# Performance work log

Hardware: AMD Instinct MI355X
Metric: run time of the kernel (lower is better)

## Reference

```python
import jax, jax.numpy as jnp
import numpy as np

N_NODES = 50000
N_EDGES = 1600000
LORA_R = 8


def gcn_conv(h, W, b, src, dst, n):
    # PyG GCNConv: linear transform, add self-loops, symmetric normalization,
    # scatter-add aggregation at target nodes, then bias.
    h = h @ W  # [N, out]
    ones = jnp.ones(src.shape[0], dtype=h.dtype)
    deg = jax.ops.segment_sum(ones, dst, num_segments=n) + 1.0  # +1 for self-loop
    dis = jax.lax.rsqrt(deg)  # deg >= 1 always
    norm = dis[src] * dis[dst]  # [E]
    agg = jax.ops.segment_sum(norm[:, None] * h[src], dst, num_segments=n)
    agg = agg + (dis * dis)[:, None] * h  # self-loop contribution
    return agg + b


def lora(h, A, B):
    # LoRALinear: b(a(x)) * (1/r); replaces input (not additive)
    return (h @ A) @ B * (1.0 / LORA_R)


def setup_inputs() -> dict:
    key = jax.random.key(0)
    ks = jax.random.split(key, 12)
    inp = {}
    inp['x'] = jax.random.normal(ks[0], (N_NODES, 128), dtype=jnp.float32)
    inp['edge_index'] = jax.random.randint(ks[1], (2, N_EDGES), 0, N_NODES, dtype=jnp.int64 if jax.config.jax_enable_x64 else jnp.int32)
    inp['domain_idx'] = jax.random.randint(ks[2], (N_NODES,), 0, 3, dtype=jnp.int32)
    inp['emb_table'] = jax.random.normal(ks[3], (3, 4096), dtype=jnp.float32)
    s1 = 1.0 / np.sqrt(4224.0)
    inp['W1'] = jax.random.normal(ks[4], (4224, 32), dtype=jnp.float32) * s1
    inp['b1'] = jnp.zeros((32,), dtype=jnp.float32)
    inp['A1'] = jax.random.normal(ks[5], (32, LORA_R), dtype=jnp.float32) * (1.0 / np.sqrt(32.0))
    inp['B1'] = jax.random.normal(ks[6], (LORA_R, 32), dtype=jnp.float32) * (1.0 / np.sqrt(LORA_R))
    inp['W2'] = jax.random.normal(ks[7], (32, 5), dtype=jnp.float32) * (1.0 / np.sqrt(32.0))
    inp['b2'] = jnp.zeros((5,), dtype=jnp.float32)
    inp['A2'] = jax.random.normal(ks[8], (5, LORA_R), dtype=jnp.float32) * (1.0 / np.sqrt(5.0))
    inp['B2'] = jax.random.normal(ks[9], (LORA_R, 5), dtype=jnp.float32) * (1.0 / np.sqrt(LORA_R))
    return inp


def reference(x, edge_index, domain_idx, emb_table, W1, b1, A1, B1, W2, b2, A2, B2):
    n = x.shape[0]
    src, dst = edge_index[0], edge_index[1]
    embedded = emb_table[domain_idx]  # [N, 4096]
    h = jnp.concatenate([embedded, x], axis=1)  # [N, 4224]
    h = gcn_conv(h, W1, b1, src, dst, n)
    h = lora(h, A1, B1)
    h = jax.nn.relu(h)
    h = gcn_conv(h, W2, b2, src, dst, n)
    h = lora(h, A2, B2)
    return jax.nn.log_softmax(h, axis=1)
```

## Files before the change

### kernel.cpp

```cpp
#include <hip/hip_runtime.h>
#include <hip/hip_bf16.h>
#include <hip/hip_fp16.h>


#define XDIM 128
#define EMBDIM 4096
#define TB 8192
#define BSH 6
#define BN 64
#define ECAP2 2560

__global__ void __launch_bounds__(256) k_bin(
    const int* __restrict__ src, const int* __restrict__ dst,
    unsigned int* __restrict__ sorted, int* __restrict__ bcur, int e, int ntiles,
    const float* __restrict__ emb, const float* __restrict__ W1,
    float* __restrict__ emb_part,
    const float* __restrict__ A1, const float* __restrict__ A2,
    const float* __restrict__ B2, const float* __restrict__ b1,
    float* __restrict__ M2, float* __restrict__ b1A1) {
    __shared__ unsigned int staged[TB];
    __shared__ int loff[1024], rctr[1024], sbase[1024];
    int t = threadIdx.x;
    if (blockIdx.x >= ntiles) {
        int bx2 = blockIdx.x - ntiles;
        int dm = bx2 >> 5, seg = bx2 & 31;
        const float* er = emb + dm * EMBDIM + seg * 128;
        const float* wr = W1 + (size_t)(seg * 128) * 32;
        int j = t & 31, kk = t >> 5;
        float acc = 0.f;
        for (int k2 = kk; k2 < 128; k2 += 8) acc += er[k2] * wr[k2 * 32 + j];
        float* p = (float*)staged;
        p[kk * 32 + j] = acc;
        __syncthreads();
        if (t < 32) {
            float s = 0.f;
            #pragma unroll
            for (int r = 0; r < 8; ++r) s += p[r * 32 + t];
            emb_part[bx2 * 32 + t] = s;
        }
        if (bx2 == 0) {
            if (t < 25) {
                int c = t / 5, cp = t % 5;
                float s = 0.f;
                #pragma unroll
                for (int r = 0; r < 8; ++r) s += A2[c * 8 + r] * B2[r * 5 + cp];
                M2[c * 5 + cp] = s * 0.125f;
            }
            if (t >= 32 && t < 40) {
                int j2 = t - 32;
                float s = 0.f;
                #pragma unroll
                for (int k = 0; k < 32; ++k) s += b1[k] * A1[k * 8 + j2];
                b1A1[j2] = s;
            }
        }
        return;
    }
    int base = blockIdx.x * TB;
    int len = min(TB, e - base);
    for (int i = t; i < 1024; i += 256) { loff[i] = 0; rctr[i] = 0; }
    __syncthreads();
    for (int i = t; i < len; i += 256) atomicAdd(&loff[dst[base + i] >> BSH], 1);
    __syncthreads();
    if (t < 64) {
        int ch = t * 16;
        int v[16]; int s0 = 0;
        #pragma unroll
        for (int k = 0; k < 16; ++k) { v[k] = loff[ch + k]; s0 += v[k]; }
        int pre = s0;
        #pragma unroll
        for (int d2 = 1; d2 < 64; d2 <<= 1) {
            int up = __shfl_up(pre, d2);
            if (t >= d2) pre += up;
        }
        int excl = pre - s0;
        #pragma unroll
        for (int k = 0; k < 16; ++k) { loff[ch + k] = excl; excl += v[k]; }
    }
    __syncthreads();
    for (int i = t; i < len; i += 256) {
        int s = src[base + i], d = dst[base + i];
        int b = d >> BSH;
        int r = atomicAdd(&rctr[b], 1);
        staged[loff[b] + r] = ((unsigned int)d << 16) | (unsigned int)s;
    }
    __syncthreads();
    for (int b2 = t; b2 < 1024; b2 += 256) {
        int l = ((b2 < 1023) ? loff[b2 + 1] : len) - loff[b2];
        if (l > 0) sbase[b2] = atomicAdd(&bcur[b2], l);
    }
    __syncthreads();
    for (int i = t; i < len; i += 256) {
        unsigned int u = staged[i];
        int b2 = (int)(u >> 22);
        int pos = sbase[b2] + (i - loff[b2]);
        if (pos < ECAP2) sorted[(size_t)b2 * ECAP2 + pos] = u;
    }
}

__global__ void __launch_bounds__(256) k_h1(
    const float* __restrict__ x, const int* __restrict__ dom,
    const float* __restrict__ emb_part, const float* __restrict__ W1,
    const float* __restrict__ A1, const unsigned int* __restrict__ sorted,
    const int* __restrict__ bcur, float* __restrict__ p1s,
    int* __restrict__ deg, unsigned short* __restrict__ nsrc, int n) {
    __shared__ float wb[XDIM * 32];
    __shared__ float xsT[XDIM * 68];
    __shared__ float sh1[64 * 33];
    __shared__ float sA1[256];
    __shared__ float sproj[96];
    __shared__ int sdom[64];
    __shared__ int hist[64], eoff[64], rctr[64];
    __shared__ unsigned short esrc[ECAP2];
    int t = threadIdx.x, b = blockIdx.x;
    int row0 = b << BSH;
    if (t < 64) { hist[t] = 0; rctr[t] = 0; }
    {
        const float4* w4 = (const float4*)(W1 + (size_t)EMBDIM * 32);
        float4* wb4 = (float4*)wb;
        for (int i = t; i < 1024; i += 256) wb4[i] = w4[i];
        sA1[t] = A1[t];
    }
    if (t < 96) {
        int d = t >> 5, j = t & 31;
        float s = 0.f;
        #pragma unroll
        for (int seg = 0; seg < 32; ++seg) s += emb_part[(d * 32 + seg) * 32 + j];
        sproj[t] = s;
    }
    if (t < 64) {
        int g = row0 + t;
        sdom[t] = (g < n) ? dom[g] * 32 : 0;
    }
    __syncthreads();
    int m = min(bcur[b], ECAP2);
    const unsigned int* sp = sorted + (size_t)b * ECAP2;
    for (int i = t; i < m; i += 256) atomicAdd(&hist[(sp[i] >> 16) & (BN - 1)], 1);
    for (int i = t; i < 2048; i += 256) {
        int row = i & 63, c4 = i >> 6;
        int g = row0 + row;
        float4 v = (g < n) ? ((const float4*)x)[(size_t)g * 32 + c4]
                           : make_float4(0.f, 0.f, 0.f, 0.f);
        int k0 = c4 * 4;
        xsT[(k0 + 0) * 68 + row] = v.x;
        xsT[(k0 + 1) * 68 + row] = v.y;
        xsT[(k0 + 2) * 68 + row] = v.z;
        xsT[(k0 + 3) * 68 + row] = v.w;
    }
    __syncthreads();
    if (t < 64) {
        int v = hist[t];
        int pre = v;
        #pragma unroll
        for (int d2 = 1; d2 < 64; d2 <<= 1) {
            int up = __shfl_up(pre, d2);
            if (t >= d2) pre += up;
        }
        eoff[t] = pre - v;
        int g = row0 + t;
        if (g < n) deg[g] = v;
    }
    int rq = t >> 4, jp = t & 15;
    float a00 = 0.f, a01 = 0.f, a10 = 0.f, a11 = 0.f;
    float a20 = 0.f, a21 = 0.f, a30 = 0.f, a31 = 0.f;
    #pragma unroll 4
    for (int k = 0; k < XDIM; ++k) {
        float4 xv = *(const float4*)(xsT + k * 68 + rq * 4);
        float2 wv = *(const float2*)(wb + k * 32 + jp * 2);
        a00 += xv.x * wv.x; a01 += xv.x * wv.y;
        a10 += xv.y * wv.x; a11 += xv.y * wv.y;
        a20 += xv.z * wv.x; a21 += xv.z * wv.y;
        a30 += xv.w * wv.x; a31 += xv.w * wv.y;
    }
    int j0 = jp * 2;
    sh1[(rq * 4 + 0) * 33 + j0]     = a00 + sproj[sdom[rq * 4 + 0] + j0];
    sh1[(rq * 4 + 0) * 33 + j0 + 1] = a01 + sproj[sdom[rq * 4 + 0] + j0 + 1];
    sh1[(rq * 4 + 1) * 33 + j0]     = a10 + sproj[sdom[rq * 4 + 1] + j0];
    sh1[(rq * 4 + 1) * 33 + j0 + 1] = a11 + sproj[sdom[rq * 4 + 1] + j0 + 1];
    sh1[(rq * 4 + 2) * 33 + j0]     = a20 + sproj[sdom[rq * 4 + 2] + j0];
    sh1[(rq * 4 + 2) * 33 + j0 + 1] = a21 + sproj[sdom[rq * 4 + 2] + j0 + 1];
    sh1[(rq * 4 + 3) * 33 + j0]     = a30 + sproj[sdom[rq * 4 + 3] + j0];
    sh1[(rq * 4 + 3) * 33 + j0 + 1] = a31 + sproj[sdom[rq * 4 + 3] + j0 + 1];
    __syncthreads();
    for (int i = t; i < m; i += 256) {
        unsigned int u = sp[i];
        int dl = (int)(u >> 16) & (BN - 1);
        int r = atomicAdd(&rctr[dl], 1);
        esrc[eoff[dl] + r] = (unsigned short)(u & 0xffffu);
    }
    for (int i = t; i < 512; i += 256) {
        int row = i >> 3, jp8 = i & 7;
        int g = row0 + row;
        if (g < n) {
            float s = 0.f;
            #pragma unroll
            for (int kk = 0; kk < 32; ++kk) s += sh1[row * 33 + kk] * sA1[kk * 8 + jp8];
            float dd = rsqrtf((float)(hist[row] + 1));
            p1s[(size_t)g * 8 + jp8] = dd * s;
        }
    }
    __syncthreads();
    {
        unsigned int* npw = (unsigned int*)(nsrc + (size_t)b * ECAP2);
        const unsigned int* ew = (const unsigned int*)esrc;
        int mw = (m + 1) >> 1;
        for (int i = t; i < mw; i += 256) npw[i] = ew[i];
    }
}

__global__ void __launch_bounds__(256) k_bagg1(
    const float* __restrict__ p1s, const unsigned short* __restrict__ nsrc,
    const int* __restrict__ bcur, const int* __restrict__ deg,
    const float* __restrict__ b1A1, const float* __restrict__ B1,
    const float* __restrict__ W2, float* __restrict__ qs, int n) {
    __shared__ unsigned short esrc[ECAP2];
    __shared__ int eoff[BN], sdeg[BN];
    __shared__ float pacc[3][BN][8];
    __shared__ float sB1[256], sW2[160], sb[8];
    int t = threadIdx.x, b = blockIdx.x;
    int node0 = b << BSH;
    sB1[t] = B1[t];
    if (t < 160) sW2[t] = W2[t];
    if (t < 8) sb[t] = b1A1[t];
    if (t < 64) {
        int node = node0 + t;
        int v = (node < n) ? deg[node] : 0;
        sdeg[t] = v;
        int pre = v;
        #pragma unroll
        for (int d2 = 1; d2 < 64; d2 <<= 1) {
            int up = __shfl_up(pre, d2);
            if (t >= d2) pre += up;
        }
        eoff[t] = pre - v;
    }
    __syncthreads();
    int m = min(bcur[b], ECAP2);
    {
        const unsigned int* npw = (const unsigned int*)(nsrc + (size_t)b * ECAP2);
        unsigned int* ew = (unsigned int*)esrc;
        int mw = (m + 1) >> 1;
        for (int i = t; i < mw; i += 256) ew[i] = npw[i];
    }
    __syncthreads();
    int nodeL = t & (BN - 1), tsub = t >> BSH;
    int base0 = eoff[nodeL], c = sdeg[nodeL];
    float a[8] = {0.f, 0.f, 0.f, 0.f, 0.f, 0.f, 0.f, 0.f};
    float a2[8] = {0.f, 0.f, 0.f, 0.f, 0.f, 0.f, 0.f, 0.f};
    int k = tsub;
    for (; k + 4 < c; k += 8) {
        int s1 = esrc[base0 + k], s2 = esrc[base0 + k + 4];
        const float4* pr1 = (const float4*)(p1s + s1 * 8);
        const float4* pr2 = (const float4*)(p1s + s2 * 8);
        float4 u0 = pr1[0], u4 = pr1[1], v0 = pr2[0], v4 = pr2[1];
        a[0] += u0.x; a[1] += u0.y; a[2] += u0.z; a[3] += u0.w;
        a[4] += u4.x; a[5] += u4.y; a[6] += u4.z; a[7] += u4.w;
        a2[0] += v0.x; a2[1] += v0.y; a2[2] += v0.z; a2[3] += v0.w;
        a2[4] += v4.x; a2[5] += v4.y; a2[6] += v4.z; a2[7] += v4.w;
    }
    for (; k < c; k += 4) {
        int s1 = esrc[base0 + k];
        const float4* pr1 = (const float4*)(p1s + s1 * 8);
        float4 u0 = pr1[0], u4 = pr1[1];
        a[0] += u0.x; a[1] += u0.y; a[2] += u0.z; a[3] += u0.w;
        a[4] += u4.x; a[5] += u4.y; a[6] += u4.z; a[7] += u4.w;
    }
    #pragma unroll
    for (int j = 0; j < 8; ++j) a[j] += a2[j];
    if (tsub > 0) {
        #pragma unroll
        for (int j = 0; j < 8; ++j) pacc[tsub - 1][nodeL][j] = a[j];
    }
    __syncthreads();
    if (t < BN) {
        int node = node0 + t;
        if (node < n) {
            float dd = rsqrtf((float)(sdeg[t] + 1));
            const float4* prn = (const float4*)(p1s + node * 8);
            float4 n0 = prn[0], n4 = prn[1];
            float af[8];
            af[0] = a[0] + n0.x; af[1] = a[1] + n0.y;
            af[2] = a[2] + n0.z; af[3] = a[3] + n0.w;
            af[4] = a[4] + n4.x; af[5] = a[5] + n4.y;
            af[6] = a[6] + n4.z; af[7] = a[7] + n4.w;
            #pragma unroll
            for (int ps = 0; ps < 3; ++ps) {
                #pragma unroll
                for (int j = 0; j < 8; ++j) af[j] += pacc[ps][t][j];
            }
            #pragma unroll
            for (int j = 0; j < 8; ++j) af[j] = dd * af[j] + sb[j];
            float qv[5] = {0.f, 0.f, 0.f, 0.f, 0.f};
            #pragma unroll
            for (int c2 = 0; c2 < 32; ++c2) {
                float tv = 0.f;
                #pragma unroll
                for (int j = 0; j < 8; ++j) tv += af[j] * sB1[j * 32 + c2];
                float st = fmaxf(tv * 0.125f, 0.f);
                #pragma unroll
                for (int o = 0; o < 5; ++o) qv[o] += st * sW2[c2 * 5 + o];
            }
            #pragma unroll
            for (int o = 0; o < 5; ++o) qs[node * 8 + o] = dd * qv[o];
        }
    }
}

__global__ void __launch_bounds__(256) k_bagg2(
    const float* __restrict__ qs, const unsigned short* __restrict__ nsrc,
    const int* __restrict__ bcur, const int* __restrict__ deg,
    const float* __restrict__ b2, const float* __restrict__ M2,
    float* __restrict__ out, int n) {
    __shared__ unsigned short esrc[ECAP2];
    __shared__ int eoff[BN], sdeg[BN];
    __shared__ float pacc[3][BN][5];
    __shared__ float sM2[25], sb2[5];
    int t = threadIdx.x, b = blockIdx.x;
    int node0 = b << BSH;
    if (t < 25) sM2[t] = M2[t];
    if (t < 5) sb2[t] = b2[t];
    if (t < 64) {
        int node = node0 + t;
        int v = (node < n) ? deg[node] : 0;
        sdeg[t] = v;
        int pre = v;
        #pragma unroll
        for (int d2 = 1; d2 < 64; d2 <<= 1) {
            int up = __shfl_up(pre, d2);
            if (t >= d2) pre += up;
        }
        eoff[t] = pre - v;
    }
    __syncthreads();
    int m = min(bcur[b], ECAP2);
    {
        const unsigned int* npw = (const unsigned int*)(nsrc + (size_t)b * ECAP2);
        unsigned int* ew = (unsigned int*)esrc;
        int mw = (m + 1) >> 1;
        for (int i = t; i < mw; i += 256) ew[i] = npw[i];
    }
    __syncthreads();
    int nodeL = t & (BN - 1), tsub = t >> BSH;
    int base0 = eoff[nodeL], c = sdeg[nodeL];
    float a[5] = {0.f, 0.f, 0.f, 0.f, 0.f};
    float a2[5] = {0.f, 0.f, 0.f, 0.f, 0.f};
    int k = tsub;
    for (; k + 4 < c; k += 8) {
        int s1 = esrc[base0 + k], s2 = esrc[base0 + k + 4];
        const float4* q1 = (const float4*)(qs + s1 * 8);
        const float4* q2 = (const float4*)(qs + s2 * 8);
        float4 u0 = q1[0]; float u4 = qs[s1 * 8 + 4];
        float4 v0 = q2[0]; float v4 = qs[s2 * 8 + 4];
        a[0] += u0.x; a[1] += u0.y; a[2] += u0.z; a[3] += u0.w; a[4] += u4;
        a2[0] += v0.x; a2[1] += v0.y; a2[2] += v0.z; a2[3] += v0.w; a2[4] += v4;
    }
    for (; k < c; k += 4) {
        int s1 = esrc[base0 + k];
        const float4* q1 = (const float4*)(qs + s1 * 8);
        float4 u0 = q1[0]; float u4 = qs[s1 * 8 + 4];
        a[0] += u0.x; a[1] += u0.y; a[2] += u0.z; a[3] += u0.w; a[4] += u4;
    }
    #pragma unroll
    for (int j = 0; j < 5; ++j) a[j] += a2[j];
    if (tsub > 0) {
        #pragma unroll
        for (int j = 0; j < 5; ++j) pacc[tsub - 1][nodeL][j] = a[j];
    }
    __syncthreads();
    if (t < BN) {
        int node = node0 + t;
        if (node < n) {
            float dd = rsqrtf((float)(sdeg[t] + 1));
            const float4* qrn = (const float4*)(qs + node * 8);
            float4 n0 = qrn[0];
            float n4 = qs[node * 8 + 4];
            float av[5];
            av[0] = a[0] + n0.x; av[1] = a[1] + n0.y; av[2] = a[2] + n0.z;
            av[3] = a[3] + n0.w; av[4] = a[4] + n4;
            #pragma unroll
            for (int ps = 0; ps < 3; ++ps) {
                #pragma unroll
                for (int j = 0; j < 5; ++j) av[j] += pacc[ps][t][j];
            }
            #pragma unroll
            for (int j = 0; j < 5; ++j) av[j] = dd * av[j] + sb2[j];
            float z[5];
            #pragma unroll
            for (int cp = 0; cp < 5; ++cp) {
                float s = 0.f;
                #pragma unroll
                for (int c2 = 0; c2 < 5; ++c2) s += av[c2] * sM2[c2 * 5 + cp];
                z[cp] = s;
            }
            float mx = z[0];
            #pragma unroll
            for (int c2 = 1; c2 < 5; ++c2) mx = fmaxf(mx, z[c2]);
            float ssum = 0.f;
            #pragma unroll
            for (int c2 = 0; c2 < 5; ++c2) ssum += __expf(z[c2] - mx);
            float ls = __logf(ssum);
            #pragma unroll
            for (int c2 = 0; c2 < 5; ++c2) out[node * 5 + c2] = z[c2] - mx - ls;
        }
    }
}

extern "C" void kernel_launch(void* const* d_in, const int* in_sizes, int n_in,
                              void* d_out, int out_size, void* d_ws, size_t ws_size,
                              hipStream_t stream) {
    const float* x   = (const float*)d_in[0];
    const int*   ei  = (const int*)d_in[1];
    const int*   dom = (const int*)d_in[2];
    const float* emb = (const float*)d_in[3];
    const float* W1  = (const float*)d_in[4];
    const float* b1  = (const float*)d_in[5];
    const float* A1  = (const float*)d_in[6];
    const float* B1  = (const float*)d_in[7];
    const float* W2  = (const float*)d_in[8];
    const float* b2  = (const float*)d_in[9];
    const float* A2  = (const float*)d_in[10];
    const float* B2  = (const float*)d_in[11];
    float* out = (float*)d_out;

    int n = in_sizes[2];
    int e = in_sizes[1] / 2;
    const int* src = ei;
    const int* dst = ei + e;

    int ntiles = (e + TB - 1) / TB;
    int nbuck  = (n + BN - 1) >> BSH;

    char* base = (char*)d_ws;
    size_t o = 0;
    auto carve = [&](size_t bytes) {
        void* p = base + o;
        o = (o + bytes + 15) & ~(size_t)15;
        return p;
    };
    float* emb_part = (float*)carve(96 * 32 * sizeof(float));
    float* M2       = (float*)carve(32 * sizeof(float));
    float* b1A1     = (float*)carve(8 * sizeof(float));
    int*   deg      = (int*)carve((size_t)n * sizeof(int));
    float* p1s      = (float*)carve((size_t)n * 8 * sizeof(float));
    float* qs       = (float*)carve((size_t)n * 8 * sizeof(float));
    int*   bcur     = (int*)carve(1024 * sizeof(int));
    unsigned int* sorted = (unsigned int*)carve((size_t)nbuck * ECAP2 * sizeof(unsigned int));
    unsigned short* nsrc = (unsigned short*)carve((size_t)nbuck * ECAP2 * sizeof(unsigned short));
    (void)ws_size; (void)n_in; (void)out_size;

    hipMemsetAsync(bcur, 0, 1024 * sizeof(int), stream);

    k_bin<<<ntiles + 96, 256, 0, stream>>>(src, dst, sorted, bcur, e, ntiles,
                                           emb, W1, emb_part, A1, A2, B2, b1, M2, b1A1);
    k_h1<<<nbuck, 256, 0, stream>>>(x, dom, emb_part, W1, A1, sorted, bcur,
                                    p1s, deg, nsrc, n);
    k_bagg1<<<nbuck, 256, 0, stream>>>(p1s, nsrc, bcur, deg, b1A1, B1, W2, qs, n);
    k_bagg2<<<nbuck, 256, 0, stream>>>(qs, nsrc, bcur, deg, b2, M2, out, n);
}
```

Measured before the change: 176.8 us.

## Store gathered node features in fp16 and compute degrees during binning

The per-node intermediate features p1 and q are now stored as fp16, which halves the bytes read by the random gathers over 1.6M edges in both aggregation kernels. Degree counting moves into the binning kernel as global atomics, so k_h1 no longer builds a per-bucket histogram. k_h1 shared memory is overlaid into one buffer, with sh1 and esrc reusing the xsT region, to cut LDS usage and a barrier. Edge-index copies are widened to uint4. The costs are reduced precision in the aggregated activations and extra global atomic traffic on deg.

```diff
diff --git a/kernel.cpp b/kernel.cpp
--- a/kernel.cpp
+++ b/kernel.cpp
@@ -12,7 +12,8 @@
 
 __global__ void __launch_bounds__(256) k_bin(
     const int* __restrict__ src, const int* __restrict__ dst,
-    unsigned int* __restrict__ sorted, int* __restrict__ bcur, int e, int ntiles,
+    unsigned int* __restrict__ sorted, int* __restrict__ bcur,
+    int* __restrict__ deg, int e, int ntiles,
     const float* __restrict__ emb, const float* __restrict__ W1,
     float* __restrict__ emb_part,
     const float* __restrict__ A1, const float* __restrict__ A2,
@@ -60,7 +61,11 @@
     int len = min(TB, e - base);
     for (int i = t; i < 1024; i += 256) { loff[i] = 0; rctr[i] = 0; }
     __syncthreads();
-    for (int i = t; i < len; i += 256) atomicAdd(&loff[dst[base + i] >> BSH], 1);
+    for (int i = t; i < len; i += 256) {
+        int d = dst[base + i];
+        atomicAdd(&loff[d >> BSH], 1);
+        atomicAdd(&deg[d], 1);
+    }
     __syncthreads();
     if (t < 64) {
         int ch = t * 16;
@@ -102,25 +107,28 @@
     const float* __restrict__ x, const int* __restrict__ dom,
     const float* __restrict__ emb_part, const float* __restrict__ W1,
     const float* __restrict__ A1, const unsigned int* __restrict__ sorted,
-    const int* __restrict__ bcur, float* __restrict__ p1s,
-    int* __restrict__ deg, unsigned short* __restrict__ nsrc, int n) {
-    __shared__ float wb[XDIM * 32];
-    __shared__ float xsT[XDIM * 68];
-    __shared__ float sh1[64 * 33];
-    __shared__ float sA1[256];
-    __shared__ float sproj[96];
-    __shared__ int sdom[64];
-    __shared__ int hist[64], eoff[64], rctr[64];
-    __shared__ unsigned short esrc[ECAP2];
+    const int* __restrict__ bcur, const int* __restrict__ deg,
+    __half* __restrict__ p1h, unsigned short* __restrict__ nsrc, int n) {
+    __shared__ __align__(16) char smem[51584];
+    float* wb   = (float*)smem;
+    float* xsT  = (float*)(smem + 16384);
+    float* sA1  = (float*)(smem + 49152);
+    float* sproj= (float*)(smem + 50176);
+    int* sdom   = (int*)(smem + 50560);
+    int* sdeg   = (int*)(smem + 50816);
+    int* eoff   = (int*)(smem + 51072);
+    int* rctr   = (int*)(smem + 51328);
+    float* sh1  = (float*)(smem + 16384);
+    unsigned short* esrc = (unsigned short*)(smem + 16384 + 8448);
+
     int t = threadIdx.x, b = blockIdx.x;
     int row0 = b << BSH;
-    if (t < 64) { hist[t] = 0; rctr[t] = 0; }
     {
         const float4* w4 = (const float4*)(W1 + (size_t)EMBDIM * 32);
         float4* wb4 = (float4*)wb;
         for (int i = t; i < 1024; i += 256) wb4[i] = w4[i];
-        sA1[t] = A1[t];
-    }
+    }
+    sA1[t] = A1[t];
     if (t < 96) {
         int d = t >> 5, j = t & 31;
         float s = 0.f;
@@ -131,47 +139,41 @@
     if (t < 64) {
         int g = row0 + t;
         sdom[t] = (g < n) ? dom[g] * 32 : 0;
-    }
-    __syncthreads();
-    int m = min(bcur[b], ECAP2);
-    const unsigned int* sp = sorted + (size_t)b * ECAP2;
-    for (int i = t; i < m; i += 256) atomicAdd(&hist[(sp[i] >> 16) & (BN - 1)], 1);
+        int v = (g < n) ? deg[g] : 0;
+        sdeg[t] = v; rctr[t] = 0;
+        int pre = v;
+        #pragma unroll
+        for (int d2 = 1; d2 < 64; d2 <<= 1) {
+            int up = __shfl_up(pre, d2);
+            if (t >= d2) pre += up;
+        }
+        eoff[t] = pre - v;
+    }
     for (int i = t; i < 2048; i += 256) {
         int row = i & 63, c4 = i >> 6;
         int g = row0 + row;
         float4 v = (g < n) ? ((const float4*)x)[(size_t)g * 32 + c4]
                            : make_float4(0.f, 0.f, 0.f, 0.f);
         int k0 = c4 * 4;
-        xsT[(k0 + 0) * 68 + row] = v.x;
-        xsT[(k0 + 1) * 68 + row] = v.y;
-        xsT[(k0 + 2) * 68 + row] = v.z;
-        xsT[(k0 + 3) * 68 + row] = v.w;
-    }
-    __syncthreads();
-    if (t < 64) {
-        int v = hist[t];
-        int pre = v;
-        #pragma unroll
-        for (int d2 = 1; d2 < 64; d2 <<= 1) {
-            int up = __shfl_up(pre, d2);
-            if (t >= d2) pre += up;
-        }
-        eoff[t] = pre - v;
-        int g = row0 + t;
-        if (g < n) deg[g] = v;
-    }
+        xsT[(k0 + 0) * 64 + row] = v.x;
+        xsT[(k0 + 1) * 64 + row] = v.y;
+        xsT[(k0 + 2) * 64 + row] = v.z;
+        xsT[(k0 + 3) * 64 + row] = v.w;
+    }
+    __syncthreads();
     int rq = t >> 4, jp = t & 15;
     float a00 = 0.f, a01 = 0.f, a10 = 0.f, a11 = 0.f;
     float a20 = 0.f, a21 = 0.f, a30 = 0.f, a31 = 0.f;
     #pragma unroll 4
     for (int k = 0; k < XDIM; ++k) {
-        float4 xv = *(const float4*)(xsT + k * 68 + rq * 4);
+        float4 xv = *(const float4*)(xsT + k * 64 + rq * 4);
         float2 wv = *(const float2*)(wb + k * 32 + jp * 2);
         a00 += xv.x * wv.x; a01 += xv.x * wv.y;
         a10 += xv.y * wv.x; a11 += xv.y * wv.y;
         a20 += xv.z * wv.x; a21 += xv.z * wv.y;
         a30 += xv.w * wv.x; a31 += xv.w * wv.y;
     }
+    __syncthreads();
     int j0 = jp * 2;
     sh1[(rq * 4 + 0) * 33 + j0]     = a00 + sproj[sdom[rq * 4 + 0] + j0];
     sh1[(rq * 4 + 0) * 33 + j0 + 1] = a01 + sproj[sdom[rq * 4 + 0] + j0 + 1];
@@ -181,13 +183,15 @@
     sh1[(rq * 4 + 2) * 33 + j0 + 1] = a21 + sproj[sdom[rq * 4 + 2] + j0 + 1];
     sh1[(rq * 4 + 3) * 33 + j0]     = a30 + sproj[sdom[rq * 4 + 3] + j0];
     sh1[(rq * 4 + 3) * 33 + j0 + 1] = a31 + sproj[sdom[rq * 4 + 3] + j0 + 1];
-    __syncthreads();
+    int m = min(bcur[b], ECAP2);
+    const unsigned int* sp = sorted + (size_t)b * ECAP2;
     for (int i = t; i < m; i += 256) {
         unsigned int u = sp[i];
         int dl = (int)(u >> 16) & (BN - 1);
         int r = atomicAdd(&rctr[dl], 1);
         esrc[eoff[dl] + r] = (unsigned short)(u & 0xffffu);
     }
+    __syncthreads();
     for (int i = t; i < 512; i += 256) {
         int row = i >> 3, jp8 = i & 7;
         int g = row0 + row;
@@ -195,25 +199,24 @@
             float s = 0.f;
             #pragma unroll
             for (int kk = 0; kk < 32; ++kk) s += sh1[row * 33 + kk] * sA1[kk * 8 + jp8];
-            float dd = rsqrtf((float)(hist[row] + 1));
-            p1s[(size_t)g * 8 + jp8] = dd * s;
-        }
-    }
-    __syncthreads();
+            float dd = rsqrtf((float)(sdeg[row] + 1));
+            p1h[(size_t)g * 8 + jp8] = __float2half_rn(dd * s);
+        }
+    }
     {
-        unsigned int* npw = (unsigned int*)(nsrc + (size_t)b * ECAP2);
-        const unsigned int* ew = (const unsigned int*)esrc;
-        int mw = (m + 1) >> 1;
+        uint4* npw = (uint4*)(nsrc + (size_t)b * ECAP2);
+        const uint4* ew = (const uint4*)esrc;
+        int mw = (m + 7) >> 3;
         for (int i = t; i < mw; i += 256) npw[i] = ew[i];
     }
 }
 
 __global__ void __launch_bounds__(256) k_bagg1(
-    const float* __restrict__ p1s, const unsigned short* __restrict__ nsrc,
+    const __half* __restrict__ p1h, const unsigned short* __restrict__ nsrc,
     const int* __restrict__ bcur, const int* __restrict__ deg,
     const float* __restrict__ b1A1, const float* __restrict__ B1,
-    const float* __restrict__ W2, float* __restrict__ qs, int n) {
-    __shared__ unsigned short esrc[ECAP2];
+    const float* __restrict__ W2, __half* __restrict__ qh, int n) {
+    __shared__ __align__(16) unsigned short esrc[ECAP2];
     __shared__ int eoff[BN], sdeg[BN];
     __shared__ float pacc[3][BN][8];
     __shared__ float sB1[256], sW2[160], sb[8];
@@ -237,9 +240,9 @@
     __syncthreads();
     int m = min(bcur[b], ECAP2);
     {
-        const unsigned int* npw = (const unsigned int*)(nsrc + (size_t)b * ECAP2);
-        unsigned int* ew = (unsigned int*)esrc;
-        int mw = (m + 1) >> 1;
+        const uint4* npw = (const uint4*)(nsrc + (size_t)b * ECAP2);
+        uint4* ew = (uint4*)esrc;
+        int mw = (m + 7) >> 3;
         for (int i = t; i < mw; i += 256) ew[i] = npw[i];
     }
     __syncthreads();
@@ -250,20 +253,26 @@
     int k = tsub;
     for (; k + 4 < c; k += 8) {
         int s1 = esrc[base0 + k], s2 = esrc[base0 + k + 4];
-        const float4* pr1 = (const float4*)(p1s + s1 * 8);
-        const float4* pr2 = (const float4*)(p1s + s2 * 8);
-        float4 u0 = pr1[0], u4 = pr1[1], v0 = pr2[0], v4 = pr2[1];
-        a[0] += u0.x; a[1] += u0.y; a[2] += u0.z; a[3] += u0.w;
-        a[4] += u4.x; a[5] += u4.y; a[6] += u4.z; a[7] += u4.w;
-        a2[0] += v0.x; a2[1] += v0.y; a2[2] += v0.z; a2[3] += v0.w;
-        a2[4] += v4.x; a2[5] += v4.y; a2[6] += v4.z; a2[7] += v4.w;
+        uint4 u = *(const uint4*)(p1h + (size_t)s1 * 8);
+        uint4 v = *(const uint4*)(p1h + (size_t)s2 * 8);
+        float2 f;
+        f = __half22float2(*(__half2*)&u.x); a[0] += f.x; a[1] += f.y;
+        f = __half22float2(*(__half2*)&u.y); a[2] += f.x; a[3] += f.y;
+        f = __half22float2(*(__half2*)&u.z); a[4] += f.x; a[5] += f.y;
+        f = __half22float2(*(__half2*)&u.w); a[6] += f.x; a[7] += f.y;
+        f = __half22float2(*(__half2*)&v.x); a2[0] += f.x; a2[1] += f.y;
+        f = __half22float2(*(__half2*)&v.y); a2[2] += f.x; a2[3] += f.y;
+        f = __half22float2(*(__half2*)&v.z); a2[4] += f.x; a2[5] += f.y;
+        f = __half22float2(*(__half2*)&v.w); a2[6] += f.x; a2[7] += f.y;
     }
     for (; k < c; k += 4) {
         int s1 = esrc[base0 + k];
-        const float4* pr1 = (const float4*)(p1s + s1 * 8);
-        float4 u0 = pr1[0], u4 = pr1[1];
-        a[0] += u0.x; a[1] += u0.y; a[2] += u0.z; a[3] += u0.w;
-        a[4] += u4.x; a[5] += u4.y; a[6] += u4.z; a[7] += u4.w;
+        uint4 u = *(const uint4*)(p1h + (size_t)s1 * 8);
+        float2 f;
+        f = __half22float2(*(__half2*)&u.x); a[0] += f.x; a[1] += f.y;
+        f = __half22float2(*(__half2*)&u.y); a[2] += f.x; a[3] += f.y;
+        f = __half22float2(*(__half2*)&u.z); a[4] += f.x; a[5] += f.y;
+        f = __half22float2(*(__half2*)&u.w); a[6] += f.x; a[7] += f.y;
     }
     #pragma unroll
     for (int j = 0; j < 8; ++j) a[j] += a2[j];
@@ -276,13 +285,13 @@
         int node = node0 + t;
         if (node < n) {
             float dd = rsqrtf((float)(sdeg[t] + 1));
-            const float4* prn = (const float4*)(p1s + node * 8);
-            float4 n0 = prn[0], n4 = prn[1];
+            uint4 u = *(const uint4*)(p1h + (size_t)node * 8);
+            float2 f;
             float af[8];
-            af[0] = a[0] + n0.x; af[1] = a[1] + n0.y;
-            af[2] = a[2] + n0.z; af[3] = a[3] + n0.w;
-            af[4] = a[4] + n4.x; af[5] = a[5] + n4.y;
-            af[6] = a[6] + n4.z; af[7] = a[7] + n4.w;
+            f = __half22float2(*(__half2*)&u.x); af[0] = a[0] + f.x; af[1] = a[1] + f.y;
+            f = __half22float2(*(__half2*)&u.y); af[2] = a[2] + f.x; af[3] = a[3] + f.y;
+            f = __half22float2(*(__half2*)&u.z); af[4] = a[4] + f.x; af[5] = a[5] + f.y;
+            f = __half22float2(*(__half2*)&u.w); af[6] = a[6] + f.x; af[7] = a[7] + f.y;
             #pragma unroll
             for (int ps = 0; ps < 3; ++ps) {
                 #pragma unroll
@@ -301,17 +310,17 @@
                 for (int o = 0; o < 5; ++o) qv[o] += st * sW2[c2 * 5 + o];
             }
             #pragma unroll
-            for (int o = 0; o < 5; ++o) qs[node * 8 + o] = dd * qv[o];
+            for (int o = 0; o < 5; ++o) qh[(size_t)node * 8 + o] = __float2half_rn(dd * qv[o]);
         }
     }
 }
 
 __global__ void __launch_bounds__(256) k_bagg2(
-    const float* __restrict__ qs, const unsigned short* __restrict__ nsrc,
+    const __half* __restrict__ qh, const unsigned short* __restrict__ nsrc,
     const int* __restrict__ bcur, const int* __restrict__ deg,
     const float* __restrict__ b2, const float* __restrict__ M2,
     float* __restrict__ out, int n) {
-    __shared__ unsigned short esrc[ECAP2];
+    __shared__ __align__(16) unsigned short esrc[ECAP2];
     __shared__ int eoff[BN], sdeg[BN];
     __shared__ float pacc[3][BN][5];
     __shared__ float sM2[25], sb2[5];
@@ -334,9 +343,9 @@
     __syncthreads();
     int m = min(bcur[b], ECAP2);
     {
-        const unsigned int* npw = (const unsigned int*)(nsrc + (size_t)b * ECAP2);
-        unsigned int* ew = (unsigned int*)esrc;
-        int mw = (m + 1) >> 1;
+        const uint4* npw = (const uint4*)(nsrc + (size_t)b * ECAP2);
+        uint4* ew = (uint4*)esrc;
+        int mw = (m + 7) >> 3;
         for (int i = t; i < mw; i += 256) ew[i] = npw[i];
     }
     __syncthreads();
@@ -347,18 +356,23 @@
     int k = tsub;
     for (; k + 4 < c; k += 8) {
         int s1 = esrc[base0 + k], s2 = esrc[base0 + k + 4];
-        const float4* q1 = (const float4*)(qs + s1 * 8);
-        const float4* q2 = (const float4*)(qs + s2 * 8);
-        float4 u0 = q1[0]; float u4 = qs[s1 * 8 + 4];
-        float4 v0 = q2[0]; float v4 = qs[s2 * 8 + 4];
-        a[0] += u0.x; a[1] += u0.y; a[2] += u0.z; a[3] += u0.w; a[4] += u4;
-        a2[0] += v0.x; a2[1] += v0.y; a2[2] += v0.z; a2[3] += v0.w; a2[4] += v4;
+        uint4 u = *(const uint4*)(qh + (size_t)s1 * 8);
+        uint4 v = *(const uint4*)(qh + (size_t)s2 * 8);
+        float2 f;
+        f = __half22float2(*(__half2*)&u.x); a[0] += f.x; a[1] += f.y;
+        f = __half22float2(*(__half2*)&u.y); a[2] += f.x; a[3] += f.y;
+        f = __half22float2(*(__half2*)&u.z); a[4] += f.x;
+        f = __half22float2(*(__half2*)&v.x); a2[0] += f.x; a2[1] += f.y;
+        f = __half22float2(*(__half2*)&v.y); a2[2] += f.x; a2[3] += f.y;
+        f = __half22float2(*(__half2*)&v.z); a2[4] += f.x;
     }
     for (; k < c; k += 4) {
         int s1 = esrc[base0 + k];
-        const float4* q1 = (const float4*)(qs + s1 * 8);
-        float4 u0 = q1[0]; float u4 = qs[s1 * 8 + 4];
-        a[0] += u0.x; a[1] += u0.y; a[2] += u0.z; a[3] += u0.w; a[4] += u4;
+        uint4 u = *(const uint4*)(qh + (size_t)s1 * 8);
+        float2 f;
+        f = __half22float2(*(__half2*)&u.x); a[0] += f.x; a[1] += f.y;
+        f = __half22float2(*(__half2*)&u.y); a[2] += f.x; a[3] += f.y;
+        f = __half22float2(*(__half2*)&u.z); a[4] += f.x;
     }
     #pragma unroll
     for (int j = 0; j < 5; ++j) a[j] += a2[j];
@@ -371,12 +385,12 @@
         int node = node0 + t;
         if (node < n) {
             float dd = rsqrtf((float)(sdeg[t] + 1));
-            const float4* qrn = (const float4*)(qs + node * 8);
-            float4 n0 = qrn[0];
-            float n4 = qs[node * 8 + 4];
+            uint4 u = *(const uint4*)(qh + (size_t)node * 8);
+            float2 f;
             float av[5];
-            av[0] = a[0] + n0.x; av[1] = a[1] + n0.y; av[2] = a[2] + n0.z;
-            av[3] = a[3] + n0.w; av[4] = a[4] + n4;
+            f = __half22float2(*(__half2*)&u.x); av[0] = a[0] + f.x; av[1] = a[1] + f.y;
+            f = __half22float2(*(__half2*)&u.y); av[2] = a[2] + f.x; av[3] = a[3] + f.y;
+            f = __half22float2(*(__half2*)&u.z); av[4] = a[4] + f.x;
             #pragma unroll
             for (int ps = 0; ps < 3; ++ps) {
                 #pragma unroll
@@ -440,20 +454,20 @@
     float* emb_part = (float*)carve(96 * 32 * sizeof(float));
     float* M2       = (float*)carve(32 * sizeof(float));
     float* b1A1     = (float*)carve(8 * sizeof(float));
+    int*   bcur     = (int*)carve(1024 * sizeof(int));
     int*   deg      = (int*)carve((size_t)n * sizeof(int));
-    float* p1s      = (float*)carve((size_t)n * 8 * sizeof(float));
-    float* qs       = (float*)carve((size_t)n * 8 * sizeof(float));
-    int*   bcur     = (int*)carve(1024 * sizeof(int));
+    __half* p1h     = (__half*)carve((size_t)n * 8 * sizeof(__half));
+    __half* qh      = (__half*)carve((size_t)n * 8 * sizeof(__half));
     unsigned int* sorted = (unsigned int*)carve((size_t)nbuck * ECAP2 * sizeof(unsigned int));
     unsigned short* nsrc = (unsigned short*)carve((size_t)nbuck * ECAP2 * sizeof(unsigned short));
     (void)ws_size; (void)n_in; (void)out_size;
 
-    hipMemsetAsync(bcur, 0, 1024 * sizeof(int), stream);
-
-    k_bin<<<ntiles + 96, 256, 0, stream>>>(src, dst, sorted, bcur, e, ntiles,
+    hipMemsetAsync(bcur, 0, 1024 * sizeof(int) + (size_t)n * sizeof(int), stream);
+
+    k_bin<<<ntiles + 96, 256, 0, stream>>>(src, dst, sorted, bcur, deg, e, ntiles,
                                            emb, W1, emb_part, A1, A2, B2, b1, M2, b1A1);
-    k_h1<<<nbuck, 256, 0, stream>>>(x, dom, emb_part, W1, A1, sorted, bcur,
-                                    p1s, deg, nsrc, n);
-    k_bagg1<<<nbuck, 256, 0, stream>>>(p1s, nsrc, bcur, deg, b1A1, B1, W2, qs, n);
-    k_bagg2<<<nbuck, 256, 0, stream>>>(qs, nsrc, bcur, deg, b2, M2, out, n);
+    k_h1<<<nbuck, 256, 0, stream>>>(x, dom, emb_part, W1, A1, sorted, bcur, deg,
+                                    p1h, nsrc, n);
+    k_bagg1<<<nbuck, 256, 0, stream>>>(p1h, nsrc, bcur, deg, b1A1, B1, W2, qh, n);
+    k_bagg2<<<nbuck, 256, 0, stream>>>(qh, nsrc, bcur, deg, b2, M2, out, n);
 }
```

Result: slower. 228.1 us (+29.0%).
